# Kernel optimization log

Hardware: AMD Instinct MI355X
Metric: run time of the kernel (lower is better)

Reference implementation:

```python
import jax, jax.numpy as jnp
import numpy as np

N_NODES = 100000
N_EDGES = 1600000
IN_FEATS = 128
HID = 32
N_REL = 5
N_BASES = 2
N_PAIRS = 4096


def setup_inputs() -> dict:
    key = jax.random.key(0)
    ks = jax.random.split(key, 24)
    d = {}
    d['x'] = jax.random.normal(ks[0], (N_NODES, IN_FEATS), dtype=jnp.float32)
    d['edge_mask'] = jnp.ones((N_EDGES,), dtype=jnp.float32)
    d['etype'] = jax.random.randint(ks[1], (N_EDGES,), 0, N_REL, dtype=jnp.int32)
    d['src'] = jax.random.randint(ks[2], (N_EDGES,), 0, N_NODES, dtype=jnp.int32)
    d['dst'] = jax.random.randint(ks[3], (N_EDGES,), 0, N_NODES, dtype=jnp.int32)
    d['users_idx'] = jax.random.randint(ks[4], (N_PAIRS,), 0, N_NODES, dtype=jnp.int32)
    d['items_idx'] = jax.random.randint(ks[5], (N_PAIRS,), 0, N_NODES, dtype=jnp.int32)
    # RelGraphConv params (basis decomposition): layer1 in->32, layers 2,3 32->32
    def s(k, din):
        return 1.0 / np.sqrt(din)
    d['V1'] = jax.random.normal(ks[6], (N_BASES, IN_FEATS, HID), dtype=jnp.float32) * s(0, IN_FEATS)
    d['comp1'] = jax.random.normal(ks[7], (N_REL, N_BASES), dtype=jnp.float32)
    d['loop1'] = jax.random.normal(ks[8], (IN_FEATS, HID), dtype=jnp.float32) * s(0, IN_FEATS)
    d['b1'] = jnp.zeros((HID,), dtype=jnp.float32)
    d['V2'] = jax.random.normal(ks[9], (N_BASES, HID, HID), dtype=jnp.float32) * s(0, HID)
    d['comp2'] = jax.random.normal(ks[10], (N_REL, N_BASES), dtype=jnp.float32)
    d['loop2'] = jax.random.normal(ks[11], (HID, HID), dtype=jnp.float32) * s(0, HID)
    d['b2'] = jnp.zeros((HID,), dtype=jnp.float32)
    d['V3'] = jax.random.normal(ks[12], (N_BASES, HID, HID), dtype=jnp.float32) * s(0, HID)
    d['comp3'] = jax.random.normal(ks[13], (N_REL, N_BASES), dtype=jnp.float32)
    d['loop3'] = jax.random.normal(ks[14], (HID, HID), dtype=jnp.float32) * s(0, HID)
    d['b3'] = jnp.zeros((HID,), dtype=jnp.float32)
    # MLP head: lin1 (2*sum(latent_dim[1:]) = 192 -> 128), lin2 (128 -> 1)
    d['w1'] = jax.random.normal(ks[15], (2 * 3 * HID, 128), dtype=jnp.float32) * (1.0 / np.sqrt(2 * 3 * HID))
    d['bw1'] = jnp.zeros((128,), dtype=jnp.float32)
    d['w2'] = jax.random.normal(ks[16], (128, 1), dtype=jnp.float32) * (1.0 / np.sqrt(128))
    d['bw2'] = jnp.zeros((1,), dtype=jnp.float32)
    return d


def _rgcn_layer(x, V, comp, loopw, bias, etype, src, dst, norm):
    # basis-decomposed relational conv: W_r = sum_b comp[r,b] * V[b]
    xb = jnp.einsum('nd,bdo->nbo', x, V)                       # [N,B,O]
    msg = jnp.einsum('eb,ebo->eo', comp[etype], xb[src])       # [E,O]
    msg = msg * norm[:, None]                                  # edge_mask norm
    agg = jax.ops.segment_sum(msg, dst, num_segments=x.shape[0])
    return jnp.tanh(agg + x @ loopw + bias)


def reference(x, edge_mask, etype, src, dst, users_idx, items_idx,
              V1, comp1, loop1, b1, V2, comp2, loop2, b2, V3, comp3, loop3, b3,
              w1, bw1, w2, bw2):
    h1 = _rgcn_layer(x, V1, comp1, loop1, b1, etype, src, dst, edge_mask)
    h2 = _rgcn_layer(h1, V2, comp2, loop2, b2, etype, src, dst, edge_mask)
    h3 = _rgcn_layer(h2, V3, comp3, loop3, b3, etype, src, dst, edge_mask)
    concat_states = jnp.concatenate([h1, h2, h3], axis=1)      # [N, 96]
    feats = jnp.concatenate([concat_states[users_idx], concat_states[items_idx]], axis=1)  # [P,192]
    hidden = jax.nn.relu(feats @ w1 + bw1)
    out = hidden @ w2 + bw2
    return out[:, 0]  # multiply_by = 1
```

## Files before the change

### kernel.cpp

```cpp
#include <hip/hip_runtime.h>
#include <stdint.h>

#define N_NODES  100000
#define N_EDGES  1600000
#define IN_FEATS 128
#define HID      32
#define N_REL    5
#define N_BASES  2
#define N_PAIRS  4096

#define NB        196
#define BCAP      16384
#define EPB       2048
#define SC_BLOCKS 782
#define TL1_BLOCKS 1250

typedef __attribute__((ext_vector_type(8))) short short8;
typedef __attribute__((ext_vector_type(4))) float f32x4;

__device__ inline unsigned int pack_bf16(float a, float b) {
    unsigned int ua = __float_as_uint(a), ub = __float_as_uint(b);
    ua = (ua + 0x7fffu + ((ua >> 16) & 1u)) >> 16;
    ub = (ub + 0x7fffu + ((ub >> 16) & 1u)) >> 16;
    return ua | (ub << 16);
}

__device__ inline unsigned short bf16_1(float a) {
    unsigned int u = __float_as_uint(a);
    u = (u + 0x7fffu + ((u >> 16) & 1u)) >> 16;
    return (unsigned short)u;
}

__device__ inline void split_bf16_2(float a, float b, unsigned int& hi, unsigned int& lo) {
    unsigned int ha = bf16_1(a), hb = bf16_1(b);
    hi = ha | (hb << 16);
    float fa = __uint_as_float(ha << 16), fb = __uint_as_float(hb << 16);
    lo = pack_bf16(a - fa, b - fb);
}


__global__ __launch_bounds__(256) void k_wprep(
    const float* __restrict__ V1, const float* __restrict__ comp1, const float* __restrict__ loop1,
    const float* __restrict__ V2, const float* __restrict__ loop2,
    const float* __restrict__ V3, const float* __restrict__ loop3,
    unsigned short* __restrict__ Wbf1, unsigned short* __restrict__ Wcat2,
    unsigned short* __restrict__ Wcat3, int* __restrict__ gcur) {
    int b = blockIdx.x;
    int t = threadIdx.x;
    if (b == 0 && t < NB) gcur[t] = 0;
    if (b < 96) {
        int idx = b * 256 + t;
        if (idx >= 192 * IN_FEATS) return;
        int j = idx / IN_FEATS, k = idx % IN_FEATS;
        float v;
        if (j < 160) {
            int r = j >> 5, o = j & 31;
            v = comp1[r * 2 + 0] * V1[(size_t)(0 * IN_FEATS + k) * 32 + o]
              + comp1[r * 2 + 1] * V1[(size_t)(1 * IN_FEATS + k) * 32 + o];
        } else {
            v = loop1[k * 32 + (j - 160)];
        }
        Wbf1[idx] = bf16_1(v);
        return;
    }
    const float *V, *loopw;
    unsigned short* Wc;
    int idx;
    if (b < 116) { V = V2; loopw = loop2; Wc = Wcat2; idx = (b - 96) * 256 + t; }
    else         { V = V3; loopw = loop3; Wc = Wcat3; idx = (b - 116) * 256 + t; }
    if (idx >= 32 * 160) return;
    int col = idx / 160, k = idx % 160;
    int seg = k >> 5, inner = k & 31;
    float v;
    if (seg < 2)      v = V[inner * 32 + col];
    else if (seg < 4) v = V[(32 + inner) * 32 + col];
    else              v = loopw[inner * 32 + col];
    Wc[idx] = bf16_1(v);
}


#define SMEM_BYTES 23856

__global__ __launch_bounds__(256) void k_fused1(
    const int* __restrict__ src, const int* __restrict__ dst,
    const int* __restrict__ etype, const float* __restrict__ mask,
    int* __restrict__ gcur, int2* __restrict__ ebuf,
    const float* __restrict__ xin,
    const unsigned short* __restrict__ Wbf, const float* __restrict__ bias,
    unsigned short* __restrict__ xs16, float* __restrict__ aggout) {
    __shared__ __attribute__((aligned(16))) char smem[SMEM_BYTES];
    int b = blockIdx.x;
    int t = threadIdx.x;
    if (b < SC_BLOCKS) {
        int2*  srec    = (int2*)smem;
        short* sb      = (short*)(smem + 16384);
        int*   lh      = (int*)(smem + 20480);
        int*   lex     = (int*)(smem + 21264);
        int*   gbase   = (int*)(smem + 22048);
        int*   scanbuf = (int*)(smem + 22832);
        int e0 = b * EPB;
        if (t < NB) lh[t] = 0;
        __syncthreads();
        int2 rec[8];
        int  bk[8];
#pragma unroll
        for (int i = 0; i < 8; i++) {
            int e = e0 + t + i * 256;
            if (e < N_EDGES) {
                int d = dst[e];
                bk[i] = d >> 9;
                rec[i].x = ((d & 511) << 23) | (src[e] << 4) | etype[e];
                rec[i].y = __float_as_int(mask[e]);
                atomicAdd(&lh[bk[i]], 1);
            } else bk[i] = -1;
        }
        __syncthreads();
        int cnt = (t < NB) ? lh[t] : 0;
        scanbuf[t] = cnt;
        __syncthreads();
        for (int off = 1; off < 256; off <<= 1) {
            int v = (t >= off) ? scanbuf[t - off] : 0;
            __syncthreads();
            scanbuf[t] += v;
            __syncthreads();
        }
        if (t < NB) {
            lex[t] = scanbuf[t] - cnt;
            gbase[t] = t * BCAP + (cnt ? atomicAdd(&gcur[t], cnt) : 0);
            lh[t] = 0;
        }
        __syncthreads();
#pragma unroll
        for (int i = 0; i < 8; i++) {
            if (bk[i] >= 0) {
                int p = lex[bk[i]] + atomicAdd(&lh[bk[i]], 1);
                srec[p] = rec[i];
                sb[p] = (short)bk[i];
            }
        }
        __syncthreads();
        int total = scanbuf[NB - 1];
        for (int idx = t; idx < total; idx += 256) {
            int bb = sb[idx];
            ebuf[gbase[bb] + (idx - lex[bb])] = srec[idx];
        }
        return;
    }
    unsigned short* As = (unsigned short*)smem;
    int bb = b - SC_BLOCKS;
    int wv = t >> 6, lane = t & 63;
    int q = lane >> 4, n16 = lane & 15;
    short8 bfr[3][4];
#pragma unroll
    for (int i = 0; i < 3; i++) {
        int tt = wv * 3 + i;
#pragma unroll
        for (int ks = 0; ks < 4; ks++)
            bfr[i][ks] = *(const short8*)(Wbf + (tt * 16 + n16) * 128 + ks * 32 + q * 8);
    }
    float bv0 = bias[n16], bv1 = bias[16 + n16];
    int node_l = t >> 4;
    int seg    = t & 15;
    int g0 = bb * 5;
#pragma unroll
    for (int gi = 0; gi < 5; gi++) {
        const float* xr = xin + ((size_t)((g0 + gi) * 16 + node_l)) * 128 + seg * 8;
        float4 p0 = *(const float4*)xr;
        float4 p1 = *(const float4*)(xr + 4);
        uint4 v;
        v.x = pack_bf16(p0.x, p0.y);
        v.y = pack_bf16(p0.z, p0.w);
        v.z = pack_bf16(p1.x, p1.y);
        v.w = pack_bf16(p1.z, p1.w);
        *(uint4*)(As + gi * 2176 + node_l * 136 + seg * 8) = v;
    }
    __syncthreads();
#pragma unroll
    for (int gi = 0; gi < 5; gi++) {
        int n0 = (g0 + gi) * 16;
        short8 afr[4];
#pragma unroll
        for (int ks = 0; ks < 4; ks++)
            afr[ks] = *(const short8*)(As + gi * 2176 + n16 * 136 + ks * 32 + q * 8);
        f32x4 d[3];
        f32x4 z = {0.f, 0.f, 0.f, 0.f};
#pragma unroll
        for (int i = 0; i < 3; i++) d[i] = z;
#pragma unroll
        for (int i = 0; i < 3; i++)
#pragma unroll
            for (int ks = 0; ks < 4; ks++)
                d[i] = __builtin_amdgcn_mfma_f32_16x16x32_bf16(afr[ks], bfr[i][ks], d[i], 0, 0, 0);
#pragma unroll
        for (int i = 0; i < 3; i++) {
            int tt = wv * 3 + i;
            if (tt < 10) {
#pragma unroll
                for (int r = 0; r < 4; r++) {
                    int node = n0 + q * 4 + r;
                    xs16[(size_t)node * 160 + tt * 16 + n16] = bf16_1(d[i][r]);
                }
            } else {
                float bv = (tt == 10) ? bv0 : bv1;
                int o = (tt - 10) * 16 + n16;
#pragma unroll
                for (int r = 0; r < 4; r++) {
                    int node = n0 + q * 4 + r;
                    aggout[(size_t)node * 32 + o] = d[i][r] + bv;
                }
            }
        }
    }
}


__global__ __launch_bounds__(512) void k_bsort2(
    const int* __restrict__ gcur, const int2* __restrict__ ebuf,
    int2* __restrict__ esort, int* __restrict__ offsets) {
    __shared__ int hist[512];
    __shared__ int incl[512];
    __shared__ int cur[512];
    __shared__ int bs[256];
    __shared__ int sBase, sCnt;
    int blk = blockIdx.x, b = blk >> 1, h = blk & 1, t = threadIdx.x;
    if (t < 256) bs[t] = (t < NB) ? gcur[t] : 0;
    __syncthreads();
    for (int off = 1; off < 256; off <<= 1) {
        int v = 0;
        if (t < 256 && t >= off) v = bs[t - off];
        __syncthreads();
        if (t < 256) bs[t] += v;
        __syncthreads();
    }
    if (t == 0) { sCnt = gcur[b]; sBase = bs[b] - gcur[b]; }
    hist[t] = 0;
    __syncthreads();
    int cnt = sCnt, gbase = sBase;
    const int2* slab = ebuf + (size_t)b * BCAP;
    for (int e = t; e < cnt; e += 512) {
        int dl = ((unsigned)slab[e].x) >> 23;
        atomicAdd(&hist[dl], 1);
    }
    __syncthreads();
    incl[t] = hist[t];
    __syncthreads();
    for (int off = 1; off < 512; off <<= 1) {
        int v = 0;
        if (t >= off) v = incl[t - off];
        __syncthreads();
        incl[t] += v;
        __syncthreads();
    }
    int ex = incl[t] - hist[t];
    cur[t] = ex;
    if ((t >> 8) == h) {
        int n = (b << 9) + t;
        if (n <= N_NODES) offsets[n] = gbase + ex;
    }
    if (b == NB - 1 && h == 1 && t == 0) offsets[N_NODES] = N_EDGES;
    __syncthreads();
    for (int e = t; e < cnt; e += 512) {
        int2 pk = slab[e];
        int dl = ((unsigned)pk.x) >> 23;
        if ((dl >> 8) == h) {
            int pos = gbase + atomicAdd(&cur[dl], 1);
            int2 rec;
            rec.x = pk.x & 0x7fffff;
            rec.y = pk.y;
            esort[pos] = rec;
        }
    }
}


__global__ __launch_bounds__(256) void k_agg1(
    const int* __restrict__ offsets, const int2* __restrict__ esort,
    const unsigned int* __restrict__ xrel16, const float* __restrict__ agg,
    float* __restrict__ concat, unsigned int* __restrict__ hrel_out) {
    int v = blockIdx.x * 32 + (threadIdx.x >> 3);
    int o = threadIdx.x & 7;
    int s0 = offsets[v], s1 = offsets[v + 1];
    float4 a0 = *(const float4*)(agg + (size_t)v * 32 + o * 4);
    float acc0 = a0.x, acc1 = a0.y, acc2 = a0.z, acc3 = a0.w;
    int last = s1 - 1;
    for (int e = s0; e < s1; e += 16) {
        int addr[16];
        float m[16];
#pragma unroll
        for (int i = 0; i < 16; i++) {
            int ei = e + i;
            int ec = (ei <= last) ? ei : last;
            int2 pk = esort[ec];
            int low = pk.x;
            addr[i] = (low >> 4) * 80 + (low & 15) * 16;
            m[i] = (ei <= last) ? __int_as_float(pk.y) : 0.f;
        }
        uint2 xw[16];
#pragma unroll
        for (int i = 0; i < 16; i++)
            xw[i] = *(const uint2*)(xrel16 + (unsigned)addr[i] + o * 2);
#pragma unroll
        for (int i = 0; i < 16; i++) {
            float f0 = __uint_as_float(xw[i].x << 16);
            float f1 = __uint_as_float(xw[i].x & 0xffff0000u);
            float f2 = __uint_as_float(xw[i].y << 16);
            float f3 = __uint_as_float(xw[i].y & 0xffff0000u);
            acc0 = fmaf(m[i], f0, acc0);
            acc1 = fmaf(m[i], f1, acc1);
            acc2 = fmaf(m[i], f2, acc2);
            acc3 = fmaf(m[i], f3, acc3);
        }
    }
    float4 r;
    r.x = tanhf(acc0); r.y = tanhf(acc1); r.z = tanhf(acc2); r.w = tanhf(acc3);
    *(float4*)(concat + (size_t)v * 96 + o * 4) = r;
    hrel_out[v * 16 + o * 2]     = pack_bf16(r.x, r.y);
    hrel_out[v * 16 + o * 2 + 1] = pack_bf16(r.z, r.w);
}


__global__ __launch_bounds__(256) void k_agg23(
    const int* __restrict__ offsets, const int2* __restrict__ esort,
    const unsigned int* __restrict__ hrel_in, const float* __restrict__ comp,
    const unsigned short* __restrict__ Wcat, const float* __restrict__ bias,
    float* __restrict__ concat, int hoff, unsigned int* __restrict__ hrel_out) {
    __shared__ unsigned int hbf[32][84];
    __shared__ float2 cLds[5];
    int t = threadIdx.x;
    if (t < 5) cLds[t] = ((const float2*)comp)[t];
    int nl = t >> 3;
    int v = blockIdx.x * 32 + nl;
    int o = t & 7;
    int s0 = offsets[v], s1 = offsets[v + 1];
    __syncthreads();
    float y00 = 0.f, y01 = 0.f, y02 = 0.f, y03 = 0.f;
    float y10 = 0.f, y11 = 0.f, y12 = 0.f, y13 = 0.f;
    int last = s1 - 1;
    for (int e = s0; e < s1; e += 16) {
        int addr[16];
        float c0[16], c1[16];
#pragma unroll
        for (int i = 0; i < 16; i++) {
            int ei = e + i;
            int ec = (ei <= last) ? ei : last;
            int2 pk = esort[ec];
            int low = pk.x;
            addr[i] = low & 0x7ffff0;
            float2 cc = cLds[low & 15];
            float m = (ei <= last) ? __int_as_float(pk.y) : 0.f;
            c0[i] = m * cc.x;
            c1[i] = m * cc.y;
        }
        uint2 xw[16];
#pragma unroll
        for (int i = 0; i < 16; i++)
            xw[i] = *(const uint2*)(hrel_in + (unsigned)addr[i] + o * 2);
#pragma unroll
        for (int i = 0; i < 16; i++) {
            float f0 = __uint_as_float(xw[i].x << 16);
            float f1 = __uint_as_float(xw[i].x & 0xffff0000u);
            float f2 = __uint_as_float(xw[i].y << 16);
            float f3 = __uint_as_float(xw[i].y & 0xffff0000u);
            y00 = fmaf(c0[i], f0, y00); y10 = fmaf(c1[i], f0, y10);
            y01 = fmaf(c0[i], f1, y01); y11 = fmaf(c1[i], f1, y11);
            y02 = fmaf(c0[i], f2, y02); y12 = fmaf(c1[i], f2, y12);
            y03 = fmaf(c0[i], f3, y03); y13 = fmaf(c1[i], f3, y13);
        }
    }
    unsigned int hi, lo;
    split_bf16_2(y00, y01, hi, lo);
    hbf[nl][o * 2]          = hi;  hbf[nl][16 + o * 2]     = lo;
    split_bf16_2(y02, y03, hi, lo);
    hbf[nl][o * 2 + 1]      = hi;  hbf[nl][16 + o * 2 + 1] = lo;
    split_bf16_2(y10, y11, hi, lo);
    hbf[nl][32 + o * 2]     = hi;  hbf[nl][48 + o * 2]     = lo;
    split_bf16_2(y12, y13, hi, lo);
    hbf[nl][32 + o * 2 + 1] = hi;  hbf[nl][48 + o * 2 + 1] = lo;
    *(uint2*)&hbf[nl][64 + o * 2] = *(const uint2*)(hrel_in + v * 16 + o * 2);
    __syncthreads();
    int wv = t >> 6, lane = t & 63;
    int q = lane >> 4, n16 = lane & 15;
    int gg = wv & 1;
    int tt = wv >> 1;
    f32x4 d = {0.f, 0.f, 0.f, 0.f};
#pragma unroll
    for (int ks = 0; ks < 5; ks++) {
        short8 afr = *(const short8*)&hbf[gg * 16 + n16][ks * 16 + q * 4];
        short8 bfr = *(const short8*)(Wcat + (tt * 16 + n16) * 160 + ks * 32 + q * 8);
        d = __builtin_amdgcn_mfma_f32_16x16x32_bf16(afr, bfr, d, 0, 0, 0);
    }
    float bv = bias[tt * 16 + n16];
    int n0 = blockIdx.x * 32 + gg * 16;
#pragma unroll
    for (int r = 0; r < 4; r++) {
        int node = n0 + q * 4 + r;
        float h = tanhf(d[r] + bv);
        concat[(size_t)node * 96 + hoff + tt * 16 + n16] = h;
        if (hrel_out)
            ((unsigned short*)hrel_out)[node * 32 + tt * 16 + n16] = bf16_1(h);
    }
}


__global__ void k_mlp(const float* __restrict__ concat, const int* __restrict__ uidx,
                      const int* __restrict__ iidx,
                      const float* __restrict__ w1, const float* __restrict__ bw1,
                      const float* __restrict__ w2, const float* __restrict__ bw2,
                      float* __restrict__ out) {
    __shared__ float feats[192];
    __shared__ float red[2];
    int p = blockIdx.x;
    int t = threadIdx.x;
    int u = uidx[p], it = iidx[p];
    for (int k = t; k < 192; k += 128)
        feats[k] = (k < 96) ? concat[(size_t)u * 96 + k] : concat[(size_t)it * 96 + (k - 96)];
    __syncthreads();
    float acc = bw1[t];
    for (int k = 0; k < 192; k++) acc += feats[k] * w1[k * 128 + t];
    float h = fmaxf(acc, 0.f);
    float part = h * w2[t];
    for (int off = 32; off > 0; off >>= 1) part += __shfl_down(part, off, 64);
    if ((t & 63) == 0) red[t >> 6] = part;
    __syncthreads();
    if (t == 0) out[p] = red[0] + red[1] + bw2[0];
}


extern "C" void kernel_launch(void* const* d_in, const int* in_sizes, int n_in,
                              void* d_out, int out_size, void* d_ws, size_t ws_size,
                              hipStream_t stream) {
    const float* x         = (const float*)d_in[0];
    const float* edge_mask = (const float*)d_in[1];
    const int*   etype     = (const int*)d_in[2];
    const int*   src       = (const int*)d_in[3];
    const int*   dst       = (const int*)d_in[4];
    const int*   users_idx = (const int*)d_in[5];
    const int*   items_idx = (const int*)d_in[6];
    const float* V1        = (const float*)d_in[7];
    const float* comp1     = (const float*)d_in[8];
    const float* loop1     = (const float*)d_in[9];
    const float* b1        = (const float*)d_in[10];
    const float* V2        = (const float*)d_in[11];
    const float* comp2     = (const float*)d_in[12];
    const float* loop2     = (const float*)d_in[13];
    const float* b2        = (const float*)d_in[14];
    const float* V3        = (const float*)d_in[15];
    const float* comp3     = (const float*)d_in[16];
    const float* loop3     = (const float*)d_in[17];
    const float* b3        = (const float*)d_in[18];
    const float* w1        = (const float*)d_in[19];
    const float* bw1       = (const float*)d_in[20];
    const float* w2        = (const float*)d_in[21];
    const float* bw2       = (const float*)d_in[22];
    float* out = (float*)d_out;

    uintptr_t w = (uintptr_t)d_ws;
    auto al = [&](size_t bytes) { uintptr_t p = (w + 255) & ~(uintptr_t)255; w = p + bytes; return p; };
    int*   gcur    = (int*)al(sizeof(int) * NB);
    int*   offsets = (int*)al(sizeof(int) * (N_NODES + 1));
    int2*  ebuf    = (int2*)al(sizeof(int2) * (size_t)NB * BCAP);
    unsigned int* xs16  = (unsigned int*)al(sizeof(unsigned int) * (size_t)N_NODES * 80);
    unsigned int* hrel1 = (unsigned int*)al(sizeof(unsigned int) * (size_t)N_NODES * 16);
    unsigned int* hrel2 = (unsigned int*)al(sizeof(unsigned int) * (size_t)N_NODES * 16);
    int2*  esort   = (int2*)al(sizeof(int2) * N_EDGES);
    unsigned short* Wbf1  = (unsigned short*)al(sizeof(unsigned short) * 192 * IN_FEATS);
    unsigned short* Wcat2 = (unsigned short*)al(sizeof(unsigned short) * 32 * 160);
    unsigned short* Wcat3 = (unsigned short*)al(sizeof(unsigned short) * 32 * 160);
    float* aggA    = (float*)al(sizeof(float) * (size_t)N_NODES * 32);
    float* concat  = (float*)al(sizeof(float) * (size_t)N_NODES * 96);

    k_wprep<<<136, 256, 0, stream>>>(V1, comp1, loop1, V2, loop2, V3, loop3,
                                     Wbf1, Wcat2, Wcat3, gcur);
    k_fused1<<<SC_BLOCKS + TL1_BLOCKS, 256, 0, stream>>>(
        src, dst, etype, edge_mask, gcur, ebuf,
        x, Wbf1, b1, (unsigned short*)xs16, aggA);
    k_bsort2<<<2 * NB, 512, 0, stream>>>(gcur, ebuf, esort, offsets);

    const int agrid = N_NODES / 32;

    k_agg1<<<agrid, 256, 0, stream>>>(offsets, esort, xs16, aggA, concat, hrel1);
    k_agg23<<<agrid, 256, 0, stream>>>(offsets, esort, hrel1, comp2, Wcat2, b2,
                                       concat, 32, hrel2);
    k_agg23<<<agrid, 256, 0, stream>>>(offsets, esort, hrel2, comp3, Wcat3, b3,
                                       concat, 64, (unsigned int*)nullptr);

    k_mlp<<<N_PAIRS, 128, 0, stream>>>(concat, users_idx, items_idx, w1, bw1, w2, bw2, out);
}
```

Baseline: 325.0 us.

## Stage layer-1 bf16 outputs in LDS and prefetch next group's inputs

The layer-1 transform path now loads one 16-node group at a time into a single LDS tile and prefetches the next group's x rows into registers while the MFMAs for the current group run. It no longer scatters 2-byte bf16 stores to global memory. The results are written to an LDS staging tile and then copied out as coalesced 16-byte row stores. This cuts LDS footprint and improves global write coalescing, at the cost of three barriers per group and the loss of full unrolling.

```diff
diff --git a/kernel.cpp b/kernel.cpp
--- a/kernel.cpp
+++ b/kernel.cpp
@@ -147,6 +147,7 @@
         return;
     }
     unsigned short* As = (unsigned short*)smem;
+    unsigned short* tb = (unsigned short*)(smem + 4352);
     int bb = b - SC_BLOCKS;
     int wv = t >> 6, lane = t & 63;
     int q = lane >> 4, n16 = lane & 15;
@@ -162,26 +163,34 @@
     int node_l = t >> 4;
     int seg    = t & 15;
     int g0 = bb * 5;
-#pragma unroll
+    float4 p0, p1;
+    {
+        const float* xr = xin + ((size_t)(g0 * 16 + node_l)) * 128 + seg * 8;
+        p0 = *(const float4*)xr;
+        p1 = *(const float4*)(xr + 4);
+    }
     for (int gi = 0; gi < 5; gi++) {
-        const float* xr = xin + ((size_t)((g0 + gi) * 16 + node_l)) * 128 + seg * 8;
-        float4 p0 = *(const float4*)xr;
-        float4 p1 = *(const float4*)(xr + 4);
-        uint4 v;
-        v.x = pack_bf16(p0.x, p0.y);
-        v.y = pack_bf16(p0.z, p0.w);
-        v.z = pack_bf16(p1.x, p1.y);
-        v.w = pack_bf16(p1.z, p1.w);
-        *(uint4*)(As + gi * 2176 + node_l * 136 + seg * 8) = v;
-    }
-    __syncthreads();
-#pragma unroll
-    for (int gi = 0; gi < 5; gi++) {
-        int n0 = (g0 + gi) * 16;
+        int g = g0 + gi;
+        int n0 = g * 16;
+        __syncthreads();
+        {
+            uint4 v;
+            v.x = pack_bf16(p0.x, p0.y);
+            v.y = pack_bf16(p0.z, p0.w);
+            v.z = pack_bf16(p1.x, p1.y);
+            v.w = pack_bf16(p1.z, p1.w);
+            *(uint4*)(As + node_l * 136 + seg * 8) = v;
+        }
+        __syncthreads();
+        if (gi + 1 < 5) {
+            const float* xr = xin + ((size_t)((g + 1) * 16 + node_l)) * 128 + seg * 8;
+            p0 = *(const float4*)xr;
+            p1 = *(const float4*)(xr + 4);
+        }
         short8 afr[4];
 #pragma unroll
         for (int ks = 0; ks < 4; ks++)
-            afr[ks] = *(const short8*)(As + gi * 2176 + n16 * 136 + ks * 32 + q * 8);
+            afr[ks] = *(const short8*)(As + n16 * 136 + ks * 32 + q * 8);
         f32x4 d[3];
         f32x4 z = {0.f, 0.f, 0.f, 0.f};
 #pragma unroll
@@ -196,10 +205,8 @@
             int tt = wv * 3 + i;
             if (tt < 10) {
 #pragma unroll
-                for (int r = 0; r < 4; r++) {
-                    int node = n0 + q * 4 + r;
-                    xs16[(size_t)node * 160 + tt * 16 + n16] = bf16_1(d[i][r]);
-                }
+                for (int r = 0; r < 4; r++)
+                    tb[(q * 4 + r) * 168 + tt * 16 + n16] = bf16_1(d[i][r]);
             } else {
                 float bv = (tt == 10) ? bv0 : bv1;
                 int o = (tt - 10) * 16 + n16;
@@ -209,6 +216,12 @@
                     aggout[(size_t)node * 32 + o] = d[i][r] + bv;
                 }
             }
+        }
+        __syncthreads();
+        for (int c = t; c < 320; c += 256) {
+            int node_i = c / 20, part = c % 20;
+            short8 vv = *(const short8*)(tb + node_i * 168 + part * 8);
+            *(short8*)(xs16 + (size_t)(n0 + node_i) * 160 + part * 8) = vv;
         }
     }
 }
```

Measured after the change: 318.8 us. Within noise of the previous version (-1.9%).
